# Optimization experiments

Hardware: AMD Instinct MI355X
Metric: run time of the kernel (lower is better)

## Reference

```python
import jax, jax.numpy as jnp
import numpy as np

N = 100000
E = 1600000
IN_F = 128
OUT_F = 128
EPS = 1e-12


def setup_inputs() -> dict:
    key = jax.random.key(0)
    k1, k2, k3, k4, k5, k6 = jax.random.split(key, 6)
    x = jax.random.normal(k1, (N, IN_F), dtype=jnp.float32)
    rows = jnp.sort(jax.random.randint(k2, (E,), 0, N, dtype=jnp.int32))
    cols = jax.random.randint(k3, (E,), 0, N, dtype=jnp.int32)
    vals = jax.random.uniform(k4, (E,), dtype=jnp.float32)
    # nn.Linear(2*in_features, out_features): W is [out, 2*in], b is [out]
    bound = 1.0 / np.sqrt(2 * IN_F)
    W = jax.random.uniform(k5, (OUT_F, 2 * IN_F), dtype=jnp.float32, minval=-bound, maxval=bound)
    b = jax.random.uniform(k6, (OUT_F,), dtype=jnp.float32, minval=-bound, maxval=bound)
    return {"x": x, "rows": rows, "cols": cols, "vals": vals, "W": W, "b": b}


def reference(x, rows, cols, vals, W, b):
    # spmm(adj, x): gather source-node features, scale by edge weight,
    # segment-sum into destination rows.
    gathered = vals[:, None] * x[cols]                      # [E, in]
    neighbor = jax.ops.segment_sum(gathered, rows, num_segments=N)  # [N, in]
    combined = jnp.concatenate([x, neighbor], axis=1)       # [N, 2*in]
    out = combined @ W.T + b                                # [N, out]
    # F.normalize(out, p=2, dim=1): divide by max(||row||_2, eps)
    norm = jnp.sqrt(jnp.sum(out * out, axis=1, keepdims=True))
    return out / jnp.maximum(norm, EPS)
```

## Files before the change

kernel.cpp:

```cpp
#include <hip/hip_runtime.h>
#include <hip/hip_bf16.h>


typedef __bf16 bf16x8_t __attribute__((ext_vector_type(8)));
typedef float f32x4_t __attribute__((ext_vector_type(4)));
typedef float f32x2_t __attribute__((ext_vector_type(2)));

__device__ __forceinline__ unsigned int f32_to_bf16(float f) {
    unsigned int u = __float_as_uint(f);
    unsigned int r = u + 0x7fffu + ((u >> 16) & 1u);
    return r >> 16;
}
__device__ __forceinline__ unsigned int pack2(float a, float b) {
    return f32_to_bf16(a) | (f32_to_bf16(b) << 16);
}
__device__ __forceinline__ float bflo(unsigned int p) { return __uint_as_float(p << 16); }
__device__ __forceinline__ float bfhi(unsigned int p) { return __uint_as_float(p & 0xffff0000u); }

__global__ void prep_kernel(const float* __restrict__ x, uint4* __restrict__ xb4,
                            const int* __restrict__ rows, int* __restrict__ row_ptr,
                            const float* __restrict__ W, uint4* __restrict__ Wf,
                            int Nn, int Ee, int xcast_blks, int rowptr_blks) {
    int blk = blockIdx.x;
    if (blk < xcast_blks) {
        int i = blk * 256 + threadIdx.x;
        if (i < Nn * 16) {
            const float4* xf = (const float4*)x;
            float4 f0 = xf[(size_t)i * 2];
            float4 f1 = xf[(size_t)i * 2 + 1];
            uint4 o;
            o.x = pack2(f0.x, f0.y); o.y = pack2(f0.z, f0.w);
            o.z = pack2(f1.x, f1.y); o.w = pack2(f1.z, f1.w);
            xb4[i] = o;
        }
    } else if (blk < xcast_blks + rowptr_blks) {
        int n = (blk - xcast_blks) * 256 + threadIdx.x;
        if (n <= Nn) {
            int lo = 0, hi = Ee;
            while (lo < hi) {
                int mid = (lo + hi) >> 1;
                if (rows[mid] < n) lo = mid + 1; else hi = mid;
            }
            row_ptr[n] = lo;
        }
    } else {
        int i = (blk - xcast_blks - rowptr_blks) * 256 + threadIdx.x;
        int lane = i & 63, ks = (i >> 6) & 7, t = i >> 9;
        int row = t * 16 + (lane & 15);
        int col = ks * 32 + (lane >> 4) * 8;
        const float* p = W + (size_t)row * 256 + col;
        uint4 o;
        o.x = pack2(p[0], p[1]); o.y = pack2(p[2], p[3]);
        o.z = pack2(p[4], p[5]); o.w = pack2(p[6], p[7]);
        Wf[i] = o;
    }
}

__global__ void fused_kernel(const int* __restrict__ row_ptr,
                             const int* __restrict__ cols,
                             const float* __restrict__ vals,
                             const char* __restrict__ xbB,
                             const bf16x8_t* __restrict__ Wf,
                             const float* __restrict__ b,
                             float* __restrict__ out, int Nn) {
    __shared__ uint4 nbLDS[16 * 17];
    __shared__ float __attribute__((aligned(16))) sqLDS[16][4];

    int lane = threadIdx.x & 63;
    int w    = threadIdx.x >> 6;

    {
        int h = lane >> 4;
        int l = lane & 15;
        int node = w * 4 + h;
        int n = blockIdx.x * 16 + node;
        int nn = min(n, Nn - 1);
        int start = row_ptr[nn], end = row_ptr[nn + 1];
        if (n >= Nn) end = start;
        unsigned loff = (unsigned)l << 4;

        f32x2_t a0 = {0.f, 0.f}, a1 = {0.f, 0.f}, a2 = {0.f, 0.f}, a3 = {0.f, 0.f};

#define EDGE4(E, C0, C1, C2, C3, V0, V1, V2, V3)                                \
        {                                                                       \
            int q0 = min((E), end - 1),     q1 = min((E) + 1, end - 1);         \
            int q2 = min((E) + 2, end - 1), q3 = min((E) + 3, end - 1);         \
            C0 = cols[q0]; C1 = cols[q1]; C2 = cols[q2]; C3 = cols[q3];         \
            V0 = ((E)     < end) ? vals[q0] : 0.f;                              \
            V1 = ((E) + 1 < end) ? vals[q1] : 0.f;                              \
            V2 = ((E) + 2 < end) ? vals[q2] : 0.f;                              \
            V3 = ((E) + 3 < end) ? vals[q3] : 0.f;                              \
        }
#define ACC(P, V)                                                               \
        {                                                                       \
            f32x2_t vv = {(V), (V)};                                            \
            f32x2_t t0 = {bflo((P).x), bfhi((P).x)};                            \
            f32x2_t t1 = {bflo((P).y), bfhi((P).y)};                            \
            f32x2_t t2 = {bflo((P).z), bfhi((P).z)};                            \
            f32x2_t t3 = {bflo((P).w), bfhi((P).w)};                            \
            a0 += vv * t0; a1 += vv * t1; a2 += vv * t2; a3 += vv * t3;         \
        }

        int e = start;
        int c0 = 0, c1 = 0, c2 = 0, c3 = 0;
        float v0 = 0.f, v1 = 0.f, v2 = 0.f, v3 = 0.f;
        if (e < end) EDGE4(e, c0, c1, c2, c3, v0, v1, v2, v3);
        while (e < end) {
            int en = e + 4;
            int d0 = 0, d1 = 0, d2 = 0, d3 = 0;
            float w0 = 0.f, w1 = 0.f, w2 = 0.f, w3 = 0.f;
            if (en < end) EDGE4(en, d0, d1, d2, d3, w0, w1, w2, w3);
            uint4 p0 = *(const uint4*)(xbB + (((unsigned)c0 << 8) | loff));
            uint4 p1 = *(const uint4*)(xbB + (((unsigned)c1 << 8) | loff));
            uint4 p2 = *(const uint4*)(xbB + (((unsigned)c2 << 8) | loff));
            uint4 p3 = *(const uint4*)(xbB + (((unsigned)c3 << 8) | loff));
            ACC(p0, v0); ACC(p1, v1); ACC(p2, v2); ACC(p3, v3);
            c0 = d0; c1 = d1; c2 = d2; c3 = d3;
            v0 = w0; v1 = w1; v2 = w2; v3 = w3;
            e = en;
        }
#undef EDGE4
#undef ACC

        uint4 o;
        o.x = pack2(a0.x, a0.y); o.y = pack2(a1.x, a1.y);
        o.z = pack2(a2.x, a2.y); o.w = pack2(a3.x, a3.y);
        nbLDS[node * 17 + l] = o;
    }
    __syncthreads();

    int m    = lane & 15;
    int quad = lane >> 4;
    int r0   = blockIdx.x * 16;

    int arow = min(r0 + m, Nn - 1);
    const bf16x8_t* Ax = (const bf16x8_t*)(xbB + (size_t)arow * 256);

    bf16x8_t a[8];
#pragma unroll
    for (int ks = 0; ks < 4; ++ks) a[ks] = Ax[ks * 4 + quad];
#pragma unroll
    for (int ks = 0; ks < 4; ++ks)
        a[4 + ks] = *(const bf16x8_t*)&nbLDS[m * 17 + ks * 4 + quad];

    f32x4_t acc[2];
    float bc[2];
#pragma unroll
    for (int j = 0; j < 2; ++j) {
        int t = w * 2 + j;
        acc[j] = (f32x4_t){0.f, 0.f, 0.f, 0.f};
        bc[j]  = b[t * 16 + m];
#pragma unroll
        for (int ks = 0; ks < 8; ++ks) {
            acc[j] = __builtin_amdgcn_mfma_f32_16x16x32_bf16(
                a[ks], Wf[(t * 8 + ks) * 64 + lane], acc[j], 0, 0, 0);
        }
    }

    float sq[4] = {0.f, 0.f, 0.f, 0.f};
#pragma unroll
    for (int j = 0; j < 2; ++j)
#pragma unroll
        for (int r = 0; r < 4; ++r) {
            float u = acc[j][r] + bc[j];
            sq[r] += u * u;
        }
#pragma unroll
    for (int off = 1; off <= 8; off <<= 1) {
#pragma unroll
        for (int r = 0; r < 4; ++r) sq[r] += __shfl_xor(sq[r], off, 64);
    }
    if (m == 0) {
#pragma unroll
        for (int r = 0; r < 4; ++r) sqLDS[quad * 4 + r][w] = sq[r];
    }
    __syncthreads();

    float scale[4];
#pragma unroll
    for (int r = 0; r < 4; ++r) {
        const float4 q4 = *(const float4*)sqLDS[quad * 4 + r];
        float tot = q4.x + q4.y + q4.z + q4.w;
        scale[r] = 1.f / fmaxf(sqrtf(tot), 1e-12f);
    }

#pragma unroll
    for (int r = 0; r < 4; ++r) {
        int row = r0 + quad * 4 + r;
        if (row < Nn) {
            float* orow = out + (size_t)row * 128;
#pragma unroll
            for (int j = 0; j < 2; ++j) {
                int t = w * 2 + j;
                orow[t * 16 + m] = (acc[j][r] + bc[j]) * scale[r];
            }
        }
    }
}

extern "C" void kernel_launch(void* const* d_in, const int* in_sizes, int n_in,
                              void* d_out, int out_size, void* d_ws, size_t ws_size,
                              hipStream_t stream) {
    const float* x    = (const float*)d_in[0];
    const int*   rows = (const int*)  d_in[1];
    const int*   cols = (const int*)  d_in[2];
    const float* vals = (const float*)d_in[3];
    const float* W    = (const float*)d_in[4];
    const float* b    = (const float*)d_in[5];
    float*       out  = (float*)d_out;

    const int Nn = in_sizes[0] / 128;
    const int Ee = in_sizes[1];

    char*  ws      = (char*)d_ws;
    int*   row_ptr = (int*)ws;
    uint4* Wf      = (uint4*)(ws + 448 * 1024);
    uint4* xb      = (uint4*)(ws + 640 * 1024);

    const int xcast_blks  = (Nn * 16 + 255) / 256;
    const int rowptr_blks = (Nn + 1 + 255) / 256;
    const int wcast_blks  = 16;

    prep_kernel<<<xcast_blks + rowptr_blks + wcast_blks, 256, 0, stream>>>(
        x, xb, rows, row_ptr, W, Wf, Nn, Ee, xcast_blks, rowptr_blks);
    fused_kernel<<<(Nn + 15) / 16, 256, 0, stream>>>(
        row_ptr, cols, vals, (const char*)xb,
        (const bf16x8_t*)Wf, b, out, Nn);
}
```

Baseline: 194.7 us.

## Software-pipeline edge gathers with deeper prefetch and wave-uniform trip count

Restructures the SpMM neighbor loop into a 4-stage register pipeline. Edge descriptors are loaded four groups ahead and x-row gathers two groups ahead, so more gather loads are in flight to hide memory latency. The trip count is made uniform across the four nodes that share a wavefront, which removes divergent loop exits. In exchange it uses more registers, which can lower occupancy, and it does wasted padded work on short rows, since the loop runs in chunks of 16 edges up to the longest row in the wave.

```diff
diff --git a/kernel.cpp b/kernel.cpp
--- a/kernel.cpp
+++ b/kernel.cpp
@@ -81,46 +81,60 @@
 
         f32x2_t a0 = {0.f, 0.f}, a1 = {0.f, 0.f}, a2 = {0.f, 0.f}, a3 = {0.f, 0.f};
 
-#define EDGE4(E, C0, C1, C2, C3, V0, V1, V2, V3)                                \
-        {                                                                       \
-            int q0 = min((E), end - 1),     q1 = min((E) + 1, end - 1);         \
-            int q2 = min((E) + 2, end - 1), q3 = min((E) + 3, end - 1);         \
-            C0 = cols[q0]; C1 = cols[q1]; C2 = cols[q2]; C3 = cols[q3];         \
-            V0 = ((E)     < end) ? vals[q0] : 0.f;                              \
-            V1 = ((E) + 1 < end) ? vals[q1] : 0.f;                              \
-            V2 = ((E) + 2 < end) ? vals[q2] : 0.f;                              \
-            V3 = ((E) + 3 < end) ? vals[q3] : 0.f;                              \
-        }
-#define ACC(P, V)                                                               \
-        {                                                                       \
-            f32x2_t vv = {(V), (V)};                                            \
-            f32x2_t t0 = {bflo((P).x), bfhi((P).x)};                            \
-            f32x2_t t1 = {bflo((P).y), bfhi((P).y)};                            \
-            f32x2_t t2 = {bflo((P).z), bfhi((P).z)};                            \
-            f32x2_t t3 = {bflo((P).w), bfhi((P).w)};                            \
-            a0 += vv * t0; a1 += vv * t1; a2 += vv * t2; a3 += vv * t3;         \
-        }
-
-        int e = start;
-        int c0 = 0, c1 = 0, c2 = 0, c3 = 0;
-        float v0 = 0.f, v1 = 0.f, v2 = 0.f, v3 = 0.f;
-        if (e < end) EDGE4(e, c0, c1, c2, c3, v0, v1, v2, v3);
-        while (e < end) {
-            int en = e + 4;
-            int d0 = 0, d1 = 0, d2 = 0, d3 = 0;
-            float w0 = 0.f, w1 = 0.f, w2 = 0.f, w3 = 0.f;
-            if (en < end) EDGE4(en, d0, d1, d2, d3, w0, w1, w2, w3);
-            uint4 p0 = *(const uint4*)(xbB + (((unsigned)c0 << 8) | loff));
-            uint4 p1 = *(const uint4*)(xbB + (((unsigned)c1 << 8) | loff));
-            uint4 p2 = *(const uint4*)(xbB + (((unsigned)c2 << 8) | loff));
-            uint4 p3 = *(const uint4*)(xbB + (((unsigned)c3 << 8) | loff));
-            ACC(p0, v0); ACC(p1, v1); ACC(p2, v2); ACC(p3, v3);
-            c0 = d0; c1 = d1; c2 = d2; c3 = d3;
-            v0 = w0; v1 = w1; v2 = w2; v3 = w3;
-            e = en;
-        }
-#undef EDGE4
-#undef ACC
+        int tg = (end - start + 3) >> 2;
+        tg = max(tg, __shfl_xor(tg, 16, 64));
+        tg = max(tg, __shfl_xor(tg, 32, 64));
+
+        int   c[4][4];
+        float v[4][4];
+        uint4 P[2][4];
+
+#define DESC(B, g) {                                                        \
+        int e0 = start + ((g) << 2);                                        \
+        int q0 = max(min(e0,     end - 1), 0);                              \
+        int q1 = max(min(e0 + 1, end - 1), 0);                              \
+        int q2 = max(min(e0 + 2, end - 1), 0);                              \
+        int q3 = max(min(e0 + 3, end - 1), 0);                              \
+        c[B][0] = cols[q0]; c[B][1] = cols[q1];                             \
+        c[B][2] = cols[q2]; c[B][3] = cols[q3];                             \
+        v[B][0] = (e0     < end) ? vals[q0] : 0.f;                          \
+        v[B][1] = (e0 + 1 < end) ? vals[q1] : 0.f;                          \
+        v[B][2] = (e0 + 2 < end) ? vals[q2] : 0.f;                          \
+        v[B][3] = (e0 + 3 < end) ? vals[q3] : 0.f;                          \
+}
+#define GATHER(PB, B) {                                                     \
+        P[PB][0] = *(const uint4*)(xbB + (((unsigned)c[B][0] << 8) | loff));\
+        P[PB][1] = *(const uint4*)(xbB + (((unsigned)c[B][1] << 8) | loff));\
+        P[PB][2] = *(const uint4*)(xbB + (((unsigned)c[B][2] << 8) | loff));\
+        P[PB][3] = *(const uint4*)(xbB + (((unsigned)c[B][3] << 8) | loff));\
+}
+#define ACC1(p, V) {                                                        \
+        f32x2_t vv = {(V), (V)};                                            \
+        f32x2_t t0 = {bflo((p).x), bfhi((p).x)};                            \
+        f32x2_t t1 = {bflo((p).y), bfhi((p).y)};                            \
+        f32x2_t t2 = {bflo((p).z), bfhi((p).z)};                            \
+        f32x2_t t3 = {bflo((p).w), bfhi((p).w)};                            \
+        a0 += vv * t0; a1 += vv * t1; a2 += vv * t2; a3 += vv * t3;         \
+}
+#define ACCG(PB, B) { ACC1(P[PB][0], v[B][0]); ACC1(P[PB][1], v[B][1]);     \
+                      ACC1(P[PB][2], v[B][2]); ACC1(P[PB][3], v[B][3]); }
+
+        DESC(0, 0); DESC(1, 1); DESC(2, 2); DESC(3, 3);
+        GATHER(0, 0);
+        GATHER(1, 1);
+
+        int nit = (tg + 3) >> 2;
+        int gb = 0;
+        for (int it = 0; it < nit; ++it, gb += 4) {
+            ACCG(0, 0);  DESC(0, gb + 4);  GATHER(0, 2);
+            ACCG(1, 1);  DESC(1, gb + 5);  GATHER(1, 3);
+            ACCG(0, 2);  DESC(2, gb + 6);  GATHER(0, 0);
+            ACCG(1, 3);  DESC(3, gb + 7);  GATHER(1, 1);
+        }
+#undef DESC
+#undef GATHER
+#undef ACC1
+#undef ACCG
 
         uint4 o;
         o.x = pack2(a0.x, a0.y); o.y = pack2(a1.x, a1.y);
```

After: 325.1 us. 67.0% more time.

## Stage edge descriptors in LDS and stream neighbor rows via async global-to-LDS ring

Applied to the files above, without the earlier changes.

Each block first copies its contiguous slice of cols/vals into shared memory, then each wave gathers neighbor feature rows with global_load_lds into a 4-deep per-wave ring buffer, waiting with vmcnt so several gathers stay in flight. This is meant to remove the dependent global index loads from the gather loop and raise memory-level parallelism. Blocks whose edge count exceeds the descriptor capacity fall back to the old register-prefetch loop. In exchange it uses more LDS, which can lower occupancy, and it relies on hand-written waitcnt ordering; each wave now iterates to the maximum degree among its four nodes, one edge per step.

```diff
diff --git a/kernel.cpp b/kernel.cpp
--- a/kernel.cpp
+++ b/kernel.cpp
@@ -5,6 +5,9 @@
 typedef __bf16 bf16x8_t __attribute__((ext_vector_type(8)));
 typedef float f32x4_t __attribute__((ext_vector_type(4)));
 typedef float f32x2_t __attribute__((ext_vector_type(2)));
+
+#define DESC_CAP 768
+#define RING_D   4
 
 __device__ __forceinline__ unsigned int f32_to_bf16(float f) {
     unsigned int u = __float_as_uint(f);
@@ -16,6 +19,14 @@
 }
 __device__ __forceinline__ float bflo(unsigned int p) { return __uint_as_float(p << 16); }
 __device__ __forceinline__ float bfhi(unsigned int p) { return __uint_as_float(p & 0xffff0000u); }
+
+__device__ __forceinline__ void gload_lds16(const char* g, void* l) {
+    auto gp = reinterpret_cast<__attribute__((address_space(1))) unsigned int*>(
+        reinterpret_cast<uintptr_t>(g));
+    auto lp = reinterpret_cast<__attribute__((address_space(3))) unsigned int*>(
+        reinterpret_cast<uintptr_t>(l));
+    __builtin_amdgcn_global_load_lds(gp, lp, 16, 0, 0);
+}
 
 __global__ void prep_kernel(const float* __restrict__ x, uint4* __restrict__ xb4,
                             const int* __restrict__ rows, int* __restrict__ row_ptr,
@@ -63,17 +74,35 @@
                              const bf16x8_t* __restrict__ Wf,
                              const float* __restrict__ b,
                              float* __restrict__ out, int Nn) {
+    __shared__ uint4 ring[4][RING_D][64];
+    __shared__ int   cLDS[DESC_CAP];
+    __shared__ float vLDS[DESC_CAP];
     __shared__ uint4 nbLDS[16 * 17];
     __shared__ float __attribute__((aligned(16))) sqLDS[16][4];
 
     int lane = threadIdx.x & 63;
     int w    = threadIdx.x >> 6;
+    int r0   = blockIdx.x * 16;
+
+    int eLo = row_ptr[r0];
+    int eHi = row_ptr[min(r0 + 16, Nn)];
+    int cnt = eHi - eLo;
+    bool big = cnt > DESC_CAP;
+
+    if (!big) {
+        for (int i = threadIdx.x; i < cnt; i += 256) {
+            cLDS[i] = cols[eLo + i];
+            vLDS[i] = vals[eLo + i];
+        }
+        if (threadIdx.x == 0 && cnt == 0) { cLDS[0] = 0; vLDS[0] = 0.f; }
+    }
+    __syncthreads();
 
     {
         int h = lane >> 4;
         int l = lane & 15;
         int node = w * 4 + h;
-        int n = blockIdx.x * 16 + node;
+        int n = r0 + node;
         int nn = min(n, Nn - 1);
         int start = row_ptr[nn], end = row_ptr[nn + 1];
         if (n >= Nn) end = start;
@@ -81,46 +110,75 @@
 
         f32x2_t a0 = {0.f, 0.f}, a1 = {0.f, 0.f}, a2 = {0.f, 0.f}, a3 = {0.f, 0.f};
 
-#define EDGE4(E, C0, C1, C2, C3, V0, V1, V2, V3)                                \
-        {                                                                       \
-            int q0 = min((E), end - 1),     q1 = min((E) + 1, end - 1);         \
-            int q2 = min((E) + 2, end - 1), q3 = min((E) + 3, end - 1);         \
-            C0 = cols[q0]; C1 = cols[q1]; C2 = cols[q2]; C3 = cols[q3];         \
-            V0 = ((E)     < end) ? vals[q0] : 0.f;                              \
-            V1 = ((E) + 1 < end) ? vals[q1] : 0.f;                              \
-            V2 = ((E) + 2 < end) ? vals[q2] : 0.f;                              \
-            V3 = ((E) + 3 < end) ? vals[q3] : 0.f;                              \
-        }
-#define ACC(P, V)                                                               \
-        {                                                                       \
-            f32x2_t vv = {(V), (V)};                                            \
-            f32x2_t t0 = {bflo((P).x), bfhi((P).x)};                            \
-            f32x2_t t1 = {bflo((P).y), bfhi((P).y)};                            \
-            f32x2_t t2 = {bflo((P).z), bfhi((P).z)};                            \
-            f32x2_t t3 = {bflo((P).w), bfhi((P).w)};                            \
-            a0 += vv * t0; a1 += vv * t1; a2 += vv * t2; a3 += vv * t3;         \
-        }
-
-        int e = start;
-        int c0 = 0, c1 = 0, c2 = 0, c3 = 0;
-        float v0 = 0.f, v1 = 0.f, v2 = 0.f, v3 = 0.f;
-        if (e < end) EDGE4(e, c0, c1, c2, c3, v0, v1, v2, v3);
-        while (e < end) {
-            int en = e + 4;
-            int d0 = 0, d1 = 0, d2 = 0, d3 = 0;
-            float w0 = 0.f, w1 = 0.f, w2 = 0.f, w3 = 0.f;
-            if (en < end) EDGE4(en, d0, d1, d2, d3, w0, w1, w2, w3);
-            uint4 p0 = *(const uint4*)(xbB + (((unsigned)c0 << 8) | loff));
-            uint4 p1 = *(const uint4*)(xbB + (((unsigned)c1 << 8) | loff));
-            uint4 p2 = *(const uint4*)(xbB + (((unsigned)c2 << 8) | loff));
-            uint4 p3 = *(const uint4*)(xbB + (((unsigned)c3 << 8) | loff));
-            ACC(p0, v0); ACC(p1, v1); ACC(p2, v2); ACC(p3, v3);
-            c0 = d0; c1 = d1; c2 = d2; c3 = d3;
-            v0 = w0; v1 = w1; v2 = w2; v3 = w3;
-            e = en;
-        }
-#undef EDGE4
-#undef ACC
+#define ACC1(p, V) {                                                        \
+        f32x2_t vv2 = {(V), (V)};                                           \
+        f32x2_t t0 = {bflo((p).x), bfhi((p).x)};                            \
+        f32x2_t t1 = {bflo((p).y), bfhi((p).y)};                            \
+        f32x2_t t2 = {bflo((p).z), bfhi((p).z)};                            \
+        f32x2_t t3 = {bflo((p).w), bfhi((p).w)};                            \
+        a0 += vv2 * t0; a1 += vv2 * t1; a2 += vv2 * t2; a3 += vv2 * t3;     \
+}
+
+        if (!big) {
+            int deg   = end - start;
+            int degm1 = deg - 1;
+            int soff  = start - eLo;
+            int tgw   = deg;
+            tgw = max(tgw, __shfl_xor(tgw, 16, 64));
+            tgw = max(tgw, __shfl_xor(tgw, 32, 64));
+
+#pragma unroll
+            for (int s = 0; s < RING_D; ++s) {
+                int idx = max(soff + min(s, degm1), 0);
+                int c = cLDS[idx];
+                gload_lds16(xbB + (((unsigned)c << 8) | loff), &ring[w][s][0]);
+            }
+
+            for (int g = 0; g < tgw; ++g) {
+                asm volatile("s_waitcnt vmcnt(3)" ::: "memory");
+                uint4 P = ring[w][g & (RING_D - 1)][lane];
+                int idxN = max(soff + min(g + RING_D, degm1), 0);
+                int cN   = cLDS[idxN];
+                int idxV = max(soff + min(g, degm1), 0);
+                float vv = vLDS[idxV];
+                if (g >= deg) vv = 0.f;
+                asm volatile("s_waitcnt lgkmcnt(0)" ::: "memory");
+                gload_lds16(xbB + (((unsigned)cN << 8) | loff),
+                            &ring[w][g & (RING_D - 1)][0]);
+                ACC1(P, vv);
+            }
+        } else {
+#define EDGE4B(E, C0, C1, C2, C3, V0, V1, V2, V3)                               \
+            {                                                                   \
+                int q0 = min((E), end - 1),     q1 = min((E) + 1, end - 1);     \
+                int q2 = min((E) + 2, end - 1), q3 = min((E) + 3, end - 1);     \
+                C0 = cols[q0]; C1 = cols[q1]; C2 = cols[q2]; C3 = cols[q3];     \
+                V0 = ((E)     < end) ? vals[q0] : 0.f;                          \
+                V1 = ((E) + 1 < end) ? vals[q1] : 0.f;                          \
+                V2 = ((E) + 2 < end) ? vals[q2] : 0.f;                          \
+                V3 = ((E) + 3 < end) ? vals[q3] : 0.f;                          \
+            }
+            int e = start;
+            int c0 = 0, c1 = 0, c2 = 0, c3 = 0;
+            float v0 = 0.f, v1 = 0.f, v2 = 0.f, v3 = 0.f;
+            if (e < end) EDGE4B(e, c0, c1, c2, c3, v0, v1, v2, v3);
+            while (e < end) {
+                int en = e + 4;
+                int d0 = 0, d1 = 0, d2 = 0, d3 = 0;
+                float w0 = 0.f, w1 = 0.f, w2 = 0.f, w3 = 0.f;
+                if (en < end) EDGE4B(en, d0, d1, d2, d3, w0, w1, w2, w3);
+                uint4 p0 = *(const uint4*)(xbB + (((unsigned)c0 << 8) | loff));
+                uint4 p1 = *(const uint4*)(xbB + (((unsigned)c1 << 8) | loff));
+                uint4 p2 = *(const uint4*)(xbB + (((unsigned)c2 << 8) | loff));
+                uint4 p3 = *(const uint4*)(xbB + (((unsigned)c3 << 8) | loff));
+                ACC1(p0, v0); ACC1(p1, v1); ACC1(p2, v2); ACC1(p3, v3);
+                c0 = d0; c1 = d1; c2 = d2; c3 = d3;
+                v0 = w0; v1 = w1; v2 = w2; v3 = w3;
+                e = en;
+            }
+#undef EDGE4B
+        }
+#undef ACC1
 
         uint4 o;
         o.x = pack2(a0.x, a0.y); o.y = pack2(a1.x, a1.y);
@@ -131,7 +189,6 @@
 
     int m    = lane & 15;
     int quad = lane >> 4;
-    int r0   = blockIdx.x * 16;
 
     int arow = min(r0 + m, Nn - 1);
     const bf16x8_t* Ax = (const bf16x8_t*)(xbB + (size_t)arow * 256);
```

After: 193.2 us. About the same (-0.7%).
